# Performance work log

Hardware: AMD Instinct MI355X
Metric: run time of the kernel (lower is better)

Reference implementation:

```python
import jax, jax.numpy as jnp
import numpy as np

MASK_VALUE = -1e6  # d2l.sequence_mask fills with -1000000.0, not -inf


def setup_inputs() -> dict:
    key = jax.random.key(0)
    kq, kk, kv, kl = jax.random.split(key, 4)
    B, Lq, Lk, D = 8, 2048, 2048, 128
    queries = jax.random.normal(kq, (B, Lq, D), dtype=jnp.float32)
    keys = jax.random.normal(kk, (B, Lk, D), dtype=jnp.float32)
    values = jax.random.normal(kv, (B, Lk, D), dtype=jnp.float32)
    valid_lens = jax.random.randint(kl, (B,), 1, Lk + 1, dtype=jnp.int32)
    return {"queries": queries, "keys": keys, "values": values, "valid_lens": valid_lens}


def reference(queries, keys, values, valid_lens):
    # scores: [B, Lq, Lk]
    d = queries.shape[-1]
    scale = 1.0 / np.sqrt(d).astype(np.float32)
    scores = jnp.einsum('bqd,bkd->bqk', queries, keys) * scale
    # 1D valid_lens -> same mask for every query row of a batch element
    mask = jnp.arange(keys.shape[1]) < valid_lens[:, None, None]  # [B,1,Lk]
    scores = jnp.where(mask, scores, MASK_VALUE)
    attn = jax.nn.softmax(scores, axis=-1)
    # dropout p=0.0 -> identity
    return jnp.einsum('bqk,bkd->bqd', attn, values)
```

## Files before the change

### kernel.cpp

```cpp
#include <hip/hip_runtime.h>
#include <hip/hip_bf16.h>
#include <hip/hip_fp16.h>

typedef __attribute__((ext_vector_type(8))) short short8;
typedef __attribute__((ext_vector_type(4))) short short4v;
typedef __attribute__((ext_vector_type(4))) float f32x4;

#define LQ     2048
#define LK     2048
#define DH     128
#define NB     8
#define KBLK   64
#define SPLITW 512
#define NSMAX  4
#define NQT64  (LQ / 64)

#define QBF_OFF (0ull)
#define KBF_OFF (4ull << 20)
#define VT_OFF  (8ull << 20)
#define OP_OFF  (12ull << 20)
#define ML_OFF  (76ull << 20)

static __device__ __forceinline__ unsigned short f2bf(float f) {
  __hip_bfloat16 h = __float2bfloat16(f);
  return __builtin_bit_cast(unsigned short, h);
}
static __device__ __forceinline__ short f2h(float f) {
  __half h = __float2half(f);
  return (short)__builtin_bit_cast(unsigned short, h);
}

#define GLDS16(gp, lp) __builtin_amdgcn_global_load_lds(                    \
    (const __attribute__((address_space(1))) void*)(gp),                    \
    (__attribute__((address_space(3))) void*)(lp), 16, 0, 0)

__global__ void __launch_bounds__(256)
prep_all(const float* __restrict__ Qg, const float* __restrict__ Kg,
         const float* __restrict__ Vg,
         unsigned short* __restrict__ Qbf, unsigned short* __restrict__ Kbf,
         unsigned short* __restrict__ Vt) {
  __shared__ unsigned short Lt[64][68];
  const int bid = blockIdx.x;
  if (bid < 2048) {
    const float SCALE = 0.08838834764831845f * 1.4426950408889634f;
    const int NQE8 = NB * LQ * DH / 8;
    int g = bid * 256 + threadIdx.x;
    const float* src;
    unsigned short* dst;
    float sc;
    int off;
    if (g < NQE8) { src = Qg; dst = Qbf; sc = SCALE; off = g * 8; }
    else          { src = Kg; dst = Kbf; sc = 1.0f;  off = (g - NQE8) * 8; }
    float4 a = *(const float4*)(src + off);
    float4 b = *(const float4*)(src + off + 4);
    short8 v;
    v[0] = (short)f2bf(a.x * sc); v[1] = (short)f2bf(a.y * sc);
    v[2] = (short)f2bf(a.z * sc); v[3] = (short)f2bf(a.w * sc);
    v[4] = (short)f2bf(b.x * sc); v[5] = (short)f2bf(b.y * sc);
    v[6] = (short)f2bf(b.z * sc); v[7] = (short)f2bf(b.w * sc);
    *(short8*)(dst + off) = v;
    return;
  }
  int vb = bid - 2048;
  int dt = vb & 1;
  int kt = (vb >> 1) & 31;
  int b  = vb >> 6;
  int t  = threadIdx.x;
  int kr = t >> 2, dc = (t & 3) * 16;
  const float* vp = Vg + (((size_t)b * LK + kt * 64 + kr) * DH + dt * 64 + dc);
#pragma unroll
  for (int j = 0; j < 4; ++j) {
    float4 x = *(const float4*)(vp + j * 4);
    Lt[kr][dc + j * 4 + 0] = f2bf(x.x);
    Lt[kr][dc + j * 4 + 1] = f2bf(x.y);
    Lt[kr][dc + j * 4 + 2] = f2bf(x.z);
    Lt[kr][dc + j * 4 + 3] = f2bf(x.w);
  }
  __syncthreads();
  int dr = t >> 2, kc = (t & 3) * 16;
  short8 w0, w1;
#pragma unroll
  for (int j = 0; j < 8; ++j) w0[j] = (short)Lt[kc + j][dr];
#pragma unroll
  for (int j = 0; j < 8; ++j) w1[j] = (short)Lt[kc + 8 + j][dr];
  unsigned short* op = Vt + (((size_t)b * DH + dt * 64 + dr) * LK + kt * 64 + kc);
  *(short8*)op = w0;
  *(short8*)(op + 8) = w1;
}

__global__ void __launch_bounds__(256, 2)
attn_split(const unsigned short* __restrict__ Qbf, const unsigned short* __restrict__ Kbf,
           const unsigned short* __restrict__ Vt, const int* __restrict__ vlens,
           __half* __restrict__ Opart, float* __restrict__ Ml) {
  const int bid   = blockIdx.x;
  const int qt    = bid & (NQT64 - 1);
  const int split = (bid >> 5) & (NSMAX - 1);
  const int b     = bid >> 7;

  const int vlen = vlens[b];
  const int kbeg = split * SPLITW;
  if (kbeg >= vlen) return;
  const int kend  = min(vlen, kbeg + SPLITW);
  const int ntile = (kend - kbeg + KBLK - 1) / KBLK;

  const int tid  = threadIdx.x;
  const int lane = tid & 63;
  const int w    = tid >> 6;
  const int l15  = lane & 15;
  const int lg   = lane >> 4;

  __shared__ __align__(16) unsigned char Kl[2][16384];
  __shared__ __align__(16) unsigned char Vl[2][16384];
  __shared__ __align__(16) unsigned char Pw[4][2048];

  const int qrow = qt * 64 + w * 16 + l15;
  const unsigned short* qp = Qbf + ((size_t)(b * LQ + qrow)) * DH;
  short8 qf[4];
#pragma unroll
  for (int dk = 0; dk < 4; ++dk) qf[dk] = *(const short8*)(qp + dk * 32 + lg * 8);

  f32x4 o[8];
#pragma unroll
  for (int i = 0; i < 8; ++i) o[i] = (f32x4){0.f, 0.f, 0.f, 0.f};
  float rm = -1e30f;
  float rl = 0.f;

  const char* Kbase = (const char*)(Kbf + (size_t)b * LK * DH);
  const char* Vbase = (const char*)(Vt + (size_t)b * DH * LK);

#define STAGE(t, bsel) do {                                                  \
    const int t0s = kbeg + (t) * KBLK;                                       \
    const char* kg_ = Kbase + (size_t)t0s * (DH * 2);                        \
    _Pragma("unroll")                                                        \
    for (int j = 0; j < 4; ++j) {                                            \
      unsigned ko_ = (unsigned)(w * 4096 + j * 1024 + lane * 16);            \
      unsigned ks_ = ko_ ^ (((ko_ >> 8) & 7u) << 4);                         \
      GLDS16(kg_ + ks_, &Kl[bsel][w * 4096 + j * 1024]);                     \
    }                                                                        \
    _Pragma("unroll")                                                        \
    for (int j = 0; j < 4; ++j) {                                            \
      unsigned vo_ = (unsigned)(w * 4096 + j * 1024 + lane * 16);            \
      unsigned d_  = vo_ >> 7;                                               \
      unsigned vs_ = (vo_ & 127u) ^ ((d_ & 7u) << 4);                        \
      const char* vg_ = Vbase + ((size_t)d_ * LK + t0s) * 2 + vs_;           \
      GLDS16(vg_, &Vl[bsel][w * 4096 + j * 1024]);                           \
    }                                                                        \
  } while (0)

  int cur = 0;
  STAGE(0, 0);
  __syncthreads();

  for (int tt = 0; tt < ntile; ++tt) {
    const int t0 = kbeg + tt * KBLK;
    if (tt + 1 < ntile) STAGE(tt + 1, cur ^ 1);

    const unsigned char* Kb = Kl[cur];
    const unsigned char* Vb = Vl[cur];

    f32x4 s[4];
#pragma unroll
    for (int ks = 0; ks < 4; ++ks) {
      f32x4 acc = (f32x4){0.f, 0.f, 0.f, 0.f};
      const int krow = ks * 16 + l15;
      const unsigned swzk = ((unsigned)(krow & 7)) << 4;
#pragma unroll
      for (int dk = 0; dk < 4; ++dk) {
        unsigned off = ((unsigned)(krow * 256 + dk * 64 + lg * 16)) ^ swzk;
        short8 kf = *(const short8*)(Kb + off);
        acc = __builtin_amdgcn_mfma_f32_16x16x32_bf16(kf, qf[dk], acc, 0, 0, 0);
      }
      s[ks] = acc;
    }

    if (t0 + KBLK > kend) {
#pragma unroll
      for (int ks = 0; ks < 4; ++ks) {
#pragma unroll
        for (int r = 0; r < 4; ++r) {
          if (t0 + ks * 16 + lg * 4 + r >= kend) s[ks][r] = -1e30f;
        }
      }
    }

    float mk[4];
#pragma unroll
    for (int ks = 0; ks < 4; ++ks)
      mk[ks] = fmaxf(fmaxf(s[ks][0], s[ks][1]), fmaxf(s[ks][2], s[ks][3]));
    float tm = fmaxf(fmaxf(mk[0], mk[1]), fmaxf(mk[2], mk[3]));
    tm = fmaxf(tm, __shfl_xor(tm, 16));
    tm = fmaxf(tm, __shfl_xor(tm, 32));
    float nm = fmaxf(rm, tm);
    float corr = exp2f(rm - nm);
    rm = nm;
#pragma unroll
    for (int ks = 0; ks < 4; ++ks) {
#pragma unroll
      for (int r = 0; r < 4; ++r) s[ks][r] = exp2f(s[ks][r] - nm);
    }

#pragma unroll
    for (int ks = 0; ks < 4; ++ks) {
      short4v wv;
      wv[0] = (short)f2bf(s[ks][0]); wv[1] = (short)f2bf(s[ks][1]);
      wv[2] = (short)f2bf(s[ks][2]); wv[3] = (short)f2bf(s[ks][3]);
      unsigned off = (unsigned)(l15 * 128 + ks * 32 + lg * 8) ^ ((unsigned)(l15 & 7) << 4);
      *(short4v*)(Pw[w] + off) = wv;
    }

#pragma unroll
    for (int dc = 0; dc < 8; ++dc) o[dc] *= corr;
    float ts = ((s[0][0] + s[0][1]) + (s[0][2] + s[0][3]))
             + ((s[1][0] + s[1][1]) + (s[1][2] + s[1][3]))
             + ((s[2][0] + s[2][1]) + (s[2][2] + s[2][3]))
             + ((s[3][0] + s[3][1]) + (s[3][2] + s[3][3]));
    ts += __shfl_xor(ts, 16);
    ts += __shfl_xor(ts, 32);
    rl = rl * corr + ts;

    short8 pa[2];
#pragma unroll
    for (int kk = 0; kk < 2; ++kk) {
      unsigned off = (unsigned)(l15 * 128 + kk * 64 + lg * 16) ^ ((unsigned)(l15 & 7) << 4);
      pa[kk] = *(const short8*)(Pw[w] + off);
    }

#pragma unroll
    for (int dc = 0; dc < 8; ++dc) {
      const int d = dc * 16 + l15;
      const unsigned swzv = ((unsigned)(d & 7)) << 4;
#pragma unroll
      for (int kk = 0; kk < 2; ++kk) {
        unsigned off = ((unsigned)(d * 128 + kk * 64 + lg * 16)) ^ swzv;
        short8 vf = *(const short8*)(Vb + off);
        o[dc] = __builtin_amdgcn_mfma_f32_16x16x32_bf16(vf, pa[kk], o[dc], 0, 0, 0);
      }
    }

    __syncthreads();
    cur ^= 1;
  }

  __half* op0 = Opart + ((size_t)(split * NB + b) * LQ + qt * 64 + w * 16) * DH;
#pragma unroll
  for (int dc = 0; dc < 8; ++dc) {
    short4v hv;
    hv[0] = f2h(o[dc][0]); hv[1] = f2h(o[dc][1]);
    hv[2] = f2h(o[dc][2]); hv[3] = f2h(o[dc][3]);
    *(short4v*)(op0 + (size_t)l15 * DH + dc * 16 + lg * 4) = hv;
  }
  if (lane < 16) {
    size_t ro = (size_t)(split * NB + b) * LQ + qt * 64 + w * 16 + lane;
    float2 ml;
    ml.x = rm;
    ml.y = rl;
    *(float2*)(Ml + ro * 2) = ml;
  }
#undef STAGE
}

__global__ void __launch_bounds__(256)
attn_combine(const __half* __restrict__ Opart, const float* __restrict__ Ml,
             const int* __restrict__ vlens, float* __restrict__ Og) {
  const int bid = blockIdx.x;
  const int q0  = bid * 2;
  const int b   = q0 >> 11;
  const int q   = (q0 & (LQ - 1)) + (threadIdx.x >> 7);
  const int d   = threadIdx.x & 127;
  const int nlive = (vlens[b] + SPLITW - 1) / SPLITW;
  float m = -1e30f;
  for (int s = 0; s < nlive; ++s)
    m = fmaxf(m, Ml[((size_t)(s * NB + b) * LQ + q) * 2]);
  float L = 0.f, acc = 0.f;
  for (int s = 0; s < nlive; ++s) {
    size_t ro = (size_t)(s * NB + b) * LQ + q;
    float w = exp2f(Ml[ro * 2] - m);
    L += w * Ml[ro * 2 + 1];
    acc += w * __half2float(Opart[ro * DH + d]);
  }
  Og[((size_t)b * LQ + q) * DH + d] = acc / L;
}

extern "C" void kernel_launch(void* const* d_in, const int* in_sizes, int n_in,
                              void* d_out, int out_size, void* d_ws, size_t ws_size,
                              hipStream_t stream) {
  const float* Q  = (const float*)d_in[0];
  const float* K  = (const float*)d_in[1];
  const float* V  = (const float*)d_in[2];
  const int*   vl = (const int*)d_in[3];
  float* O = (float*)d_out;

  unsigned short* Qbf = (unsigned short*)((char*)d_ws + QBF_OFF);
  unsigned short* Kbf = (unsigned short*)((char*)d_ws + KBF_OFF);
  unsigned short* Vt  = (unsigned short*)((char*)d_ws + VT_OFF);
  __half* Opart = (__half*)((char*)d_ws + OP_OFF);
  float* Ml     = (float*)((char*)d_ws + ML_OFF);

  hipLaunchKernelGGL(prep_all, dim3(2560), dim3(256), 0, stream, Q, K, V, Qbf, Kbf, Vt);
  hipLaunchKernelGGL(attn_split, dim3(NB * NSMAX * NQT64), dim3(256), 0, stream,
                     Qbf, Kbf, Vt, vl, Opart, Ml);
  hipLaunchKernelGGL(attn_combine, dim3(NB * LQ / 2), dim3(256), 0, stream,
                     Opart, Ml, vl, O);
}
```

Before: 50.44 us.

## Replace double-buffered LDS-direct loads with register-staged single-buffer prefetch

```diff
diff --git a/kernel.cpp b/kernel.cpp
--- a/kernel.cpp
+++ b/kernel.cpp
@@ -29,10 +29,6 @@
   __half h = __float2half(f);
   return (short)__builtin_bit_cast(unsigned short, h);
 }
-
-#define GLDS16(gp, lp) __builtin_amdgcn_global_load_lds(                    \
-    (const __attribute__((address_space(1))) void*)(gp),                    \
-    (__attribute__((address_space(3))) void*)(lp), 16, 0, 0)
 
 __global__ void __launch_bounds__(256)
 prep_all(const float* __restrict__ Qg, const float* __restrict__ Kg,
@@ -88,7 +84,7 @@
   *(short8*)(op + 8) = w1;
 }
 
-__global__ void __launch_bounds__(256, 2)
+__global__ void __launch_bounds__(256, 4)
 attn_split(const unsigned short* __restrict__ Qbf, const unsigned short* __restrict__ Kbf,
            const unsigned short* __restrict__ Vt, const int* __restrict__ vlens,
            __half* __restrict__ Opart, float* __restrict__ Ml) {
@@ -109,8 +105,8 @@
   const int l15  = lane & 15;
   const int lg   = lane >> 4;
 
-  __shared__ __align__(16) unsigned char Kl[2][16384];
-  __shared__ __align__(16) unsigned char Vl[2][16384];
+  __shared__ __align__(16) unsigned char Kl[16384];
+  __shared__ __align__(16) unsigned char Vl[16384];
   __shared__ __align__(16) unsigned char Pw[4][2048];
 
   const int qrow = qt * 64 + w * 16 + l15;
@@ -128,35 +124,46 @@
   const char* Kbase = (const char*)(Kbf + (size_t)b * LK * DH);
   const char* Vbase = (const char*)(Vt + (size_t)b * DH * LK);
 
-#define STAGE(t, bsel) do {                                                  \
+  unsigned ldst[4], ksrc[4];
+  size_t vsrc[4];
+#pragma unroll
+  for (int j = 0; j < 4; ++j) {
+    unsigned ko = (unsigned)(w * 4096 + j * 1024 + lane * 16);
+    ldst[j] = ko;
+    ksrc[j] = ko ^ (((ko >> 8) & 7u) << 4);
+    unsigned d_ = ko >> 7;
+    unsigned vs = (ko & 127u) ^ ((d_ & 7u) << 4);
+    vsrc[j] = (size_t)d_ * (LK * 2) + vs;
+  }
+
+  f32x4 kreg[4], vreg[4];
+
+#define RLOAD(t) do {                                                        \
     const int t0s = kbeg + (t) * KBLK;                                       \
     const char* kg_ = Kbase + (size_t)t0s * (DH * 2);                        \
+    const char* vg_ = Vbase + (size_t)t0s * 2;                               \
     _Pragma("unroll")                                                        \
     for (int j = 0; j < 4; ++j) {                                            \
-      unsigned ko_ = (unsigned)(w * 4096 + j * 1024 + lane * 16);            \
-      unsigned ks_ = ko_ ^ (((ko_ >> 8) & 7u) << 4);                         \
-      GLDS16(kg_ + ks_, &Kl[bsel][w * 4096 + j * 1024]);                     \
+      kreg[j] = *(const f32x4*)(kg_ + ksrc[j]);                              \
+      vreg[j] = *(const f32x4*)(vg_ + vsrc[j]);                              \
     }                                                                        \
+  } while (0)
+
+#define WLDS() do {                                                          \
     _Pragma("unroll")                                                        \
     for (int j = 0; j < 4; ++j) {                                            \
-      unsigned vo_ = (unsigned)(w * 4096 + j * 1024 + lane * 16);            \
-      unsigned d_  = vo_ >> 7;                                               \
-      unsigned vs_ = (vo_ & 127u) ^ ((d_ & 7u) << 4);                        \
-      const char* vg_ = Vbase + ((size_t)d_ * LK + t0s) * 2 + vs_;           \
-      GLDS16(vg_, &Vl[bsel][w * 4096 + j * 1024]);                           \
+      *(f32x4*)(&Kl[ldst[j]]) = kreg[j];                                     \
+      *(f32x4*)(&Vl[ldst[j]]) = vreg[j];                                     \
     }                                                                        \
   } while (0)
 
-  int cur = 0;
-  STAGE(0, 0);
+  RLOAD(0);
+  WLDS();
   __syncthreads();
 
   for (int tt = 0; tt < ntile; ++tt) {
     const int t0 = kbeg + tt * KBLK;
-    if (tt + 1 < ntile) STAGE(tt + 1, cur ^ 1);
-
-    const unsigned char* Kb = Kl[cur];
-    const unsigned char* Vb = Vl[cur];
+    if (tt + 1 < ntile) RLOAD(tt + 1);
 
     f32x4 s[4];
 #pragma unroll
@@ -167,7 +174,7 @@
 #pragma unroll
       for (int dk = 0; dk < 4; ++dk) {
         unsigned off = ((unsigned)(krow * 256 + dk * 64 + lg * 16)) ^ swzk;
-        short8 kf = *(const short8*)(Kb + off);
+        short8 kf = *(const short8*)(Kl + off);
         acc = __builtin_amdgcn_mfma_f32_16x16x32_bf16(kf, qf[dk], acc, 0, 0, 0);
       }
       s[ks] = acc;
@@ -232,13 +239,16 @@
 #pragma unroll
       for (int kk = 0; kk < 2; ++kk) {
         unsigned off = ((unsigned)(d * 128 + kk * 64 + lg * 16)) ^ swzv;
-        short8 vf = *(const short8*)(Vb + off);
+        short8 vf = *(const short8*)(Vl + off);
         o[dc] = __builtin_amdgcn_mfma_f32_16x16x32_bf16(vf, pa[kk], o[dc], 0, 0, 0);
       }
     }
 
-    __syncthreads();
-    cur ^= 1;
+    if (tt + 1 < ntile) {
+      __syncthreads();
+      WLDS();
+      __syncthreads();
+    }
   }
 
   __half* op0 = Opart + ((size_t)(split * NB + b) * LQ + qt * 64 + w * 16) * DH;
@@ -256,7 +266,8 @@
     ml.y = rl;
     *(float2*)(Ml + ro * 2) = ml;
   }
-#undef STAGE
+#undef RLOAD
+#undef WLDS
 }
 
 __global__ void __launch_bounds__(256)
```

Result: slower. 100.4 us (+99.0%).

## Fuse Q bf16 conversion into attention kernel and skip K/V prep past valid length

Applied to the files above, without the earlier changes.

```diff
diff --git a/kernel.cpp b/kernel.cpp
--- a/kernel.cpp
+++ b/kernel.cpp
@@ -15,7 +15,6 @@
 #define NSMAX  4
 #define NQT64  (LQ / 64)
 
-#define QBF_OFF (0ull)
 #define KBF_OFF (4ull << 20)
 #define VT_OFF  (8ull << 20)
 #define OP_OFF  (12ull << 20)
@@ -35,36 +34,33 @@
     (__attribute__((address_space(3))) void*)(lp), 16, 0, 0)
 
 __global__ void __launch_bounds__(256)
-prep_all(const float* __restrict__ Qg, const float* __restrict__ Kg,
-         const float* __restrict__ Vg,
-         unsigned short* __restrict__ Qbf, unsigned short* __restrict__ Kbf,
-         unsigned short* __restrict__ Vt) {
+prep_kv(const float* __restrict__ Kg, const float* __restrict__ Vg,
+        const int* __restrict__ vlens,
+        unsigned short* __restrict__ Kbf, unsigned short* __restrict__ Vt) {
   __shared__ unsigned short Lt[64][68];
   const int bid = blockIdx.x;
-  if (bid < 2048) {
-    const float SCALE = 0.08838834764831845f * 1.4426950408889634f;
-    const int NQE8 = NB * LQ * DH / 8;
+  if (bid < 1024) {
+    const int b      = bid >> 7;
+    const int row0   = (bid & 127) * 16;
+    const int kceil  = (vlens[b] + 63) & ~63;
+    if (row0 >= kceil) return;
     int g = bid * 256 + threadIdx.x;
-    const float* src;
-    unsigned short* dst;
-    float sc;
-    int off;
-    if (g < NQE8) { src = Qg; dst = Qbf; sc = SCALE; off = g * 8; }
-    else          { src = Kg; dst = Kbf; sc = 1.0f;  off = (g - NQE8) * 8; }
-    float4 a = *(const float4*)(src + off);
-    float4 b = *(const float4*)(src + off + 4);
+    int off = g * 8;
+    float4 a = *(const float4*)(Kg + off);
+    float4 c = *(const float4*)(Kg + off + 4);
     short8 v;
-    v[0] = (short)f2bf(a.x * sc); v[1] = (short)f2bf(a.y * sc);
-    v[2] = (short)f2bf(a.z * sc); v[3] = (short)f2bf(a.w * sc);
-    v[4] = (short)f2bf(b.x * sc); v[5] = (short)f2bf(b.y * sc);
-    v[6] = (short)f2bf(b.z * sc); v[7] = (short)f2bf(b.w * sc);
-    *(short8*)(dst + off) = v;
+    v[0] = (short)f2bf(a.x); v[1] = (short)f2bf(a.y);
+    v[2] = (short)f2bf(a.z); v[3] = (short)f2bf(a.w);
+    v[4] = (short)f2bf(c.x); v[5] = (short)f2bf(c.y);
+    v[6] = (short)f2bf(c.z); v[7] = (short)f2bf(c.w);
+    *(short8*)(Kbf + off) = v;
     return;
   }
-  int vb = bid - 2048;
+  int vb = bid - 1024;
   int dt = vb & 1;
   int kt = (vb >> 1) & 31;
   int b  = vb >> 6;
+  if (kt * 64 >= vlens[b]) return;
   int t  = threadIdx.x;
   int kr = t >> 2, dc = (t & 3) * 16;
   const float* vp = Vg + (((size_t)b * LK + kt * 64 + kr) * DH + dt * 64 + dc);
@@ -89,7 +85,7 @@
 }
 
 __global__ void __launch_bounds__(256, 2)
-attn_split(const unsigned short* __restrict__ Qbf, const unsigned short* __restrict__ Kbf,
+attn_split(const float* __restrict__ Qg, const unsigned short* __restrict__ Kbf,
            const unsigned short* __restrict__ Vt, const int* __restrict__ vlens,
            __half* __restrict__ Opart, float* __restrict__ Ml) {
   const int bid   = blockIdx.x;
@@ -113,11 +109,19 @@
   __shared__ __align__(16) unsigned char Vl[2][16384];
   __shared__ __align__(16) unsigned char Pw[4][2048];
 
+  const float SCALE = 0.08838834764831845f * 1.4426950408889634f;
   const int qrow = qt * 64 + w * 16 + l15;
-  const unsigned short* qp = Qbf + ((size_t)(b * LQ + qrow)) * DH;
+  const float* qpf = Qg + ((size_t)(b * LQ + qrow)) * DH;
   short8 qf[4];
 #pragma unroll
-  for (int dk = 0; dk < 4; ++dk) qf[dk] = *(const short8*)(qp + dk * 32 + lg * 8);
+  for (int dk = 0; dk < 4; ++dk) {
+    float4 x = *(const float4*)(qpf + dk * 32 + lg * 8);
+    float4 y = *(const float4*)(qpf + dk * 32 + lg * 8 + 4);
+    qf[dk][0] = (short)f2bf(x.x * SCALE); qf[dk][1] = (short)f2bf(x.y * SCALE);
+    qf[dk][2] = (short)f2bf(x.z * SCALE); qf[dk][3] = (short)f2bf(x.w * SCALE);
+    qf[dk][4] = (short)f2bf(y.x * SCALE); qf[dk][5] = (short)f2bf(y.y * SCALE);
+    qf[dk][6] = (short)f2bf(y.z * SCALE); qf[dk][7] = (short)f2bf(y.w * SCALE);
+  }
 
   f32x4 o[8];
 #pragma unroll
@@ -290,15 +294,14 @@
   const int*   vl = (const int*)d_in[3];
   float* O = (float*)d_out;
 
-  unsigned short* Qbf = (unsigned short*)((char*)d_ws + QBF_OFF);
   unsigned short* Kbf = (unsigned short*)((char*)d_ws + KBF_OFF);
   unsigned short* Vt  = (unsigned short*)((char*)d_ws + VT_OFF);
   __half* Opart = (__half*)((char*)d_ws + OP_OFF);
   float* Ml     = (float*)((char*)d_ws + ML_OFF);
 
-  hipLaunchKernelGGL(prep_all, dim3(2560), dim3(256), 0, stream, Q, K, V, Qbf, Kbf, Vt);
+  hipLaunchKernelGGL(prep_kv, dim3(1536), dim3(256), 0, stream, K, V, vl, Kbf, Vt);
   hipLaunchKernelGGL(attn_split, dim3(NB * NSMAX * NQT64), dim3(256), 0, stream,
-                     Qbf, Kbf, Vt, vl, Opart, Ml);
+                     Q, Kbf, Vt, vl, Opart, Ml);
   hipLaunchKernelGGL(attn_combine, dim3(NB * LQ / 2), dim3(256), 0, stream,
                      Opart, Ml, vl, O);
 }
```

Measured after the change: 50.42 us. About the same (-0.1%).
